# Optimization experiments

Hardware: AMD Instinct MI355X
Metric: run time of the kernel (lower is better)

## Reference

```python
import jax, jax.numpy as jnp
import numpy as np

OBJECTNESS_LIMIT = 0.7
MIN_SIZE = 10.0
N_ANCHORS = 9  # 3 aspects x 3 scales from RPN.anchors


def _conv(x, w, padding):
    return jax.lax.conv_general_dilated(
        x, w, window_strides=(1, 1), padding=padding,
        dimension_numbers=('NHWC', 'HWIO', 'NHWC'))


def setup_inputs() -> dict:
    key = jax.random.key(0)
    ks = jax.random.split(key, 7)
    B, H, W, C = 8, 64, 64, 512
    data = jax.random.normal(ks[0], (B, H, W, C), dtype=jnp.float32)
    # base 3x3 conv 512->256 ('normal' init), relu
    w_base = jax.random.normal(ks[1], (3, 3, C, 256), dtype=jnp.float32) * 0.05
    b_base = jnp.zeros((256,), dtype=jnp.float32)
    # classifier 1x1 conv 256->9 ('uniform' init), sigmoid
    w_cls = jax.random.uniform(ks[2], (1, 1, 256, N_ANCHORS), dtype=jnp.float32,
                               minval=-0.05, maxval=0.05)
    b_cls = jnp.zeros((N_ANCHORS,), dtype=jnp.float32)
    # branch is exercised / gradients flow)
    w_reg = jax.random.normal(ks[3], (1, 1, 256, N_ANCHORS * 4), dtype=jnp.float32) * 0.05
    b_reg = jnp.zeros((N_ANCHORS * 4,), dtype=jnp.float32)
    return {'data': data, 'w_base': w_base, 'b_base': b_base,
            'w_cls': w_cls, 'b_cls': b_cls, 'w_reg': w_reg, 'b_reg': b_reg}


def reference(data, w_base, b_base, w_cls, b_cls, w_reg, b_reg):
    # RPN base conv: 3x3, same padding, relu
    feat = jax.nn.relu(_conv(data, w_base, 'SAME') + b_base)        # [B,H,W,256]
    obj = jax.nn.sigmoid(_conv(feat, w_cls, 'VALID') + b_cls)       # [B,H,W,9]
    boxes = _conv(feat, w_reg, 'VALID') + b_reg                     # [B,H,W,36]
    B, H, W, _ = boxes.shape
    boxes = boxes.reshape(B, H, W, N_ANCHORS, 4)
    mask = (obj > OBJECTNESS_LIMIT) & (boxes[..., 2] > MIN_SIZE) & (boxes[..., 3] > MIN_SIZE)
    # boxes failing selection are dropped (yielded as None) -> zeroed here
    boxes = jnp.where(mask[..., None], boxes, jnp.zeros((), boxes.dtype))
    # objectness is always emitted; pack (boxes, objectness) densely
    out = jnp.concatenate([boxes.reshape(B, H, W, N_ANCHORS * 4), obj], axis=-1)  # [B,H,W,45]
    return out
```

## Files before the change

kernel.cpp:

```cpp
#include <hip/hip_runtime.h>
#include <hip/hip_bf16.h>

typedef unsigned short u16;
typedef unsigned int   u32;

typedef __attribute__((ext_vector_type(8))) short bfrag;
typedef __attribute__((ext_vector_type(4))) float f32x4;

static __device__ __forceinline__ u16 f2bf(float f) {
    u32 u = __float_as_uint(f);
    return (u16)((u + 0x7fffu + ((u >> 16) & 1u)) >> 16);
}
static __device__ __forceinline__ u32 pk2(float a, float b) {
    return (u32)f2bf(a) | ((u32)f2bf(b) << 16);
}
static __device__ __forceinline__ float bf2f(u16 h) {
    return __uint_as_float((u32)h << 16);
}

#define AS1 __attribute__((address_space(1)))
#define AS3 __attribute__((address_space(3)))
static __device__ __forceinline__ void gload_lds16(const u16* g, u16* l) {
    __builtin_amdgcn_global_load_lds((const AS1 u32*)g, (AS3 u32*)l, 16, 0, 0);
}

__global__ __launch_bounds__(256) void prep_w_k(const float* __restrict__ wb,
                                                u16* __restrict__ wt)
{
    int i  = blockIdx.x * 256 + threadIdx.x;
    int ci = i & 511;
    int co = (i >> 9) & 255;
    int pos = i >> 17;
    wt[i] = f2bf(wb[(size_t)((pos << 9) + ci) * 256 + co]);
}

__global__ __launch_bounds__(256) void prep_hw_k(const float* __restrict__ wc,
                                                 const float* __restrict__ wr,
                                                 u16* __restrict__ wh)
{
    int i = blockIdx.x * 256 + threadIdx.x;
    int ch = i >> 8, c = i & 255;
    float v = 0.f;
    if (ch < 36)      v = wr[c * 36 + ch];
    else if (ch < 45) v = wc[c * 9 + ch - 36];
    wh[i] = f2bf(v);
}

__global__ __launch_bounds__(256) void prep_a_k(const float* __restrict__ data,
                                                u16* __restrict__ abf)
{
    int gid = blockIdx.x * 256 + threadIdx.x;
    int ch8 = gid & 63;
    int row = gid >> 6;
    int img = row / 4356;
    int rem = row - img * 4356;
    int py  = rem / 66;
    int px  = rem - py * 66;
    uint4 o;
    if (py == 0 || py == 65 || px == 0 || px == 65) {
        o = make_uint4(0u, 0u, 0u, 0u);
    } else {
        const float4* s = (const float4*)(data +
            ((size_t)((img << 12) + ((py - 1) << 6) + (px - 1)) << 9) + (ch8 << 3));
        float4 v0 = s[0], v1 = s[1];
        o = make_uint4(pk2(v0.x, v0.y), pk2(v0.z, v0.w),
                       pk2(v1.x, v1.y), pk2(v1.z, v1.w));
    }
    *(uint4*)(abf + ((size_t)row << 9) + (ch8 << 3)) = o;
}

__global__ __launch_bounds__(256, 2) void gemm_k(
    const u16*   __restrict__ abf,
    const u16*   __restrict__ wt,
    const float* __restrict__ bb,
    u16*         __restrict__ feat)
{
    __shared__ u16 As[128 * 64];
    __shared__ u16 Bs[128 * 64];

    int bid = blockIdx.x;
    int wg  = ((bid & 7) << 6) | (bid >> 3);
    int mt  = wg >> 1, nt = wg & 1;
    int pm0 = mt << 7, cn0 = nt << 7;
    int img = mt >> 5;
    int y0  = (mt & 31) << 1;

    int tid = threadIdx.x, lane = tid & 63, w = tid >> 6;
    int wm2 = (w >> 1) << 6, wn2 = (w & 1) << 6;
    int fr = lane & 15, fg = lane >> 4;

    const u16* pA[4]; const u16* pB[4];
    int ldsOff[4];
    #pragma unroll
    for (int i = 0; i < 4; ++i) {
        int slot = i * 256 + w * 64 + lane;
        int row  = slot >> 3, g = slot & 7;
        int gs   = g ^ (row & 7);
        int y = y0 + (row >> 6), x = row & 63;
        pA[i] = abf + ((size_t)((img * 66 + y) * 66 + x) << 9) + (gs << 3);
        pB[i] = wt  + ((size_t)(cn0 + row) << 9) + (gs << 3);
        ldsOff[i] = (i * 256 + w * 64) << 3;
    }

    int aoff[2][4], boff[2][4];
    #pragma unroll
    for (int kk = 0; kk < 2; ++kk)
        #pragma unroll
        for (int t = 0; t < 4; ++t) {
            int ra = wm2 + (t << 4) + fr;
            int rb = wn2 + (t << 4) + fr;
            int q  = (kk << 2) | fg;
            aoff[kk][t] = (ra << 6) + ((q ^ (ra & 7)) << 3);
            boff[kk][t] = (rb << 6) + ((q ^ (rb & 7)) << 3);
        }

    f32x4 acc[4][4] = {};

    #pragma unroll 1
    for (int pos = 0; pos < 9; ++pos) {
        int py = pos / 3, px = pos % 3;
        size_t aEl = ((size_t)(py * 66 + px)) << 9;
        size_t bEl = ((size_t)pos) << 17;
        #pragma unroll 1
        for (int cb = 0; cb < 8; ++cb) {
            size_t soA = aEl + (cb << 6);
            size_t soB = bEl + (cb << 6);
            #pragma unroll
            for (int i = 0; i < 4; ++i) gload_lds16(pA[i] + soA, &As[ldsOff[i]]);
            #pragma unroll
            for (int i = 0; i < 4; ++i) gload_lds16(pB[i] + soB, &Bs[ldsOff[i]]);
            __syncthreads();

            #pragma unroll
            for (int kk = 0; kk < 2; ++kk) {
                bfrag av[4], bv[4];
                #pragma unroll
                for (int t = 0; t < 4; ++t) {
                    av[t] = *(const bfrag*)&As[aoff[kk][t]];
                    bv[t] = *(const bfrag*)&Bs[boff[kk][t]];
                }
                #pragma unroll
                for (int mi = 0; mi < 4; ++mi)
                    #pragma unroll
                    for (int ni = 0; ni < 4; ++ni)
                        acc[mi][ni] = __builtin_amdgcn_mfma_f32_16x16x32_bf16(
                            av[mi], bv[ni], acc[mi][ni], 0, 0, 0);
            }
            __syncthreads();
        }
    }

    #pragma unroll
    for (int ni = 0; ni < 4; ++ni) {
        int co = cn0 + wn2 + (ni << 4) + fr;
        float bias = bb[co];
        #pragma unroll
        for (int mi = 0; mi < 4; ++mi) {
            int pixb = pm0 + wm2 + (mi << 4) + (fg << 2);
            #pragma unroll
            for (int r = 0; r < 4; ++r) {
                float v = fmaxf(acc[mi][ni][r] + bias, 0.f);
                feat[(size_t)(pixb + r) * 256 + co] = f2bf(v);
            }
        }
    }
}

__global__ __launch_bounds__(256, 2) void head_k(
    const u16*   __restrict__ feat,
    const u16*   __restrict__ wh,
    const float* __restrict__ bc,
    const float* __restrict__ br,
    float*       __restrict__ out)
{
    __shared__ union {
        u16   ft[64 * 256];
        float raw[64 * 45];
    } sm;

    int bid = blockIdx.x;
    int wg  = ((bid & 7) << 6) | (bid >> 3);
    int pb  = wg << 6;

    int tid = threadIdx.x, lane = tid & 63, w = tid >> 6;
    int fr = lane & 15, fg = lane >> 4;
    int wm = w << 4;

    bfrag bv[3][8];
    #pragma unroll
    for (int nt = 0; nt < 3; ++nt)
        #pragma unroll
        for (int kk = 0; kk < 8; ++kk)
            bv[nt][kk] = *(const bfrag*)(wh + ((nt << 4) + fr) * 256 + (kk << 5) + (fg << 3));

    const u16* fbase = feat + ((size_t)pb << 8);
    #pragma unroll
    for (int i = 0; i < 8; ++i) {
        int slot = i * 256 + tid;
        int row  = slot >> 5, g = slot & 31;
        int gs   = g ^ (row & 7);
        gload_lds16(fbase + (row << 8) + (gs << 3), &sm.ft[(i * 256 + w * 64) << 3]);
    }
    __syncthreads();

    f32x4 acc[3] = {};
    #pragma unroll
    for (int kk = 0; kk < 8; ++kk) {
        int row = wm + fr;
        int ga  = (kk << 2) | fg;
        bfrag av = *(const bfrag*)&sm.ft[(row << 8) + ((ga ^ (row & 7)) << 3)];
        #pragma unroll
        for (int nt = 0; nt < 3; ++nt)
            acc[nt] = __builtin_amdgcn_mfma_f32_16x16x32_bf16(av, bv[nt][kk], acc[nt], 0, 0, 0);
    }
    __syncthreads();

    #pragma unroll
    for (int nt = 0; nt < 3; ++nt) {
        int ch = (nt << 4) + fr;
        if (ch < 45) {
            float bias = (ch < 36) ? br[ch] : bc[ch - 36];
            int pix = wm + (fg << 2);
            #pragma unroll
            for (int r = 0; r < 4; ++r)
                sm.raw[(pix + r) * 45 + ch] = acc[nt][r] + bias;
        }
    }
    __syncthreads();

    {
        int pix = tid >> 2, q = tid & 3;
        const float* rp = &sm.raw[pix * 45];
        float* op = out + (size_t)(pb + pix) * 45;
        int na = (q == 3) ? 3 : 2;
        int a0 = (q == 3) ? 6 : (q << 1);
        for (int t = 0; t < na; ++t) {
            int a = a0 + t;
            float lg  = rp[36 + a];
            float obj = 1.f / (1.f + __expf(-lg));
            float b0 = rp[4*a], b1 = rp[4*a+1], b2 = rp[4*a+2], b3 = rp[4*a+3];
            bool m = (obj > 0.7f) && (b2 > 10.f) && (b3 > 10.f);
            op[4*a    ] = m ? b0 : 0.f;
            op[4*a + 1] = m ? b1 : 0.f;
            op[4*a + 2] = m ? b2 : 0.f;
            op[4*a + 3] = m ? b3 : 0.f;
            op[36 + a ] = obj;
        }
    }
}

union FbSmem {
    u16   hal[3 * 66 * 64];
    u16   ft[256][64];
    float raw[64 * 45];
};

template<int WMODE>
__global__ __launch_bounds__(256, 2) void fb_k(
    const float* __restrict__ data, const u16* __restrict__ wt,
    const float* __restrict__ wb, const float* __restrict__ bb,
    const float* __restrict__ wc, const float* __restrict__ bc,
    const float* __restrict__ wr, const float* __restrict__ br,
    float* __restrict__ out)
{
    __shared__ FbSmem sm;
    int bid = blockIdx.x;
    int wg  = ((bid & 7) << 6) | (bid >> 3);
    int pm0 = wg << 6;
    int img = wg >> 6;
    int y0  = wg & 63;
    int tid = threadIdx.x, lane = tid & 63, wid = tid >> 6;
    int wn = wid << 6;
    int fr = lane & 15, fg = lane >> 4;
    f32x4 acc[4][4] = {};

    #pragma unroll 1
    for (int cb = 0; cb < 8; ++cb) {
        __syncthreads();
        #pragma unroll
        for (int t = 0; t < 3; ++t) {
            int lin = t * 256 + tid;
            int row = lin >> 8, col = (lin >> 2) & 63, cq = lin & 3;
            int sy = y0 + row - 1;
            bool ok = (sy >= 0) && (sy < 64);
            float4 v0, v1, v2, v3;
            if (ok) {
                const float4* s = (const float4*)(data +
                    ((size_t)((img << 12) + (sy << 6) + col) << 9) + (cb << 6) + (cq << 4));
                v0 = s[0]; v1 = s[1]; v2 = s[2]; v3 = s[3];
            } else { v0 = v1 = v2 = v3 = make_float4(0.f, 0.f, 0.f, 0.f); }
            int hc = col + 1;
            u16* base = &sm.hal[(row * 66 + hc) << 6];
            int g0 = ((cq << 1) | 0) ^ (hc & 7);
            int g1 = ((cq << 1) | 1) ^ (hc & 7);
            *(uint4*)&base[g0 << 3] = make_uint4(pk2(v0.x,v0.y), pk2(v0.z,v0.w),
                                                 pk2(v1.x,v1.y), pk2(v1.z,v1.w));
            *(uint4*)&base[g1 << 3] = make_uint4(pk2(v2.x,v2.y), pk2(v2.z,v2.w),
                                                 pk2(v3.x,v3.y), pk2(v3.z,v3.w));
        }
        if (tid < 48) {
            int zr = tid >> 4, zrem = tid & 15;
            int zc = (zrem >> 3) ? 65 : 0, zg = zrem & 7;
            *(uint4*)&sm.hal[(((zr * 66 + zc) << 3) | zg) << 3] = make_uint4(0,0,0,0);
        }
        __syncthreads();

        #pragma unroll
        for (int pos = 0; pos < 9; ++pos) {
            int dy = pos / 3 - 1, dx = pos % 3 - 1;
            bfrag bv[2][4];
            if (WMODE == 0) {
                #pragma unroll
                for (int kk = 0; kk < 2; ++kk)
                    #pragma unroll
                    for (int i = 0; i < 4; ++i)
                        bv[kk][i] = *(const bfrag*)(wt + ((size_t)pos << 17) +
                            ((size_t)(wn + (i << 4) + fr) << 9) + (cb << 6) +
                            (kk << 5) + (fg << 3));
            } else {
                #pragma unroll
                for (int kk = 0; kk < 2; ++kk)
                    #pragma unroll
                    for (int i = 0; i < 4; ++i) {
                        int co = wn + (i << 4) + fr;
                        const float* s = wb +
                            (size_t)((pos << 9) + (cb << 6) + (kk << 5) + (fg << 3)) * 256 + co;
                        union { short sh[8]; bfrag v; } tb;
                        #pragma unroll
                        for (int j = 0; j < 8; ++j) tb.sh[j] = (short)f2bf(s[(size_t)j << 8]);
                        bv[kk][i] = tb.v;
                    }
            }
            int hr = dy + 1;
            bfrag av[2][4];
            #pragma unroll
            for (int kk = 0; kk < 2; ++kk)
                #pragma unroll
                for (int i = 0; i < 4; ++i) {
                    int hc = (i << 4) + fr + dx + 1;
                    int g  = ((kk << 2) | fg) ^ (hc & 7);
                    av[kk][i] = *(const bfrag*)&sm.hal[(((hr * 66 + hc) << 3) | g) << 3];
                }
            #pragma unroll
            for (int kk = 0; kk < 2; ++kk)
                #pragma unroll
                for (int mi = 0; mi < 4; ++mi)
                    #pragma unroll
                    for (int ni = 0; ni < 4; ++ni)
                        acc[mi][ni] = __builtin_amdgcn_mfma_f32_16x16x32_bf16(
                            av[kk][mi], bv[kk][ni], acc[mi][ni], 0, 0, 0);
        }
    }
    __syncthreads();

    #pragma unroll
    for (int ni = 0; ni < 4; ++ni) {
        int co = wn + (ni << 4) + fr;
        float bias = bb[co];
        int rot = (co & 15) << 2;
        #pragma unroll
        for (int mi = 0; mi < 4; ++mi) {
            int pb  = (mi << 4) + (fg << 2);
            int col = (pb + rot) & 63;
            float r0 = fmaxf(acc[mi][ni][0] + bias, 0.f);
            float r1 = fmaxf(acc[mi][ni][1] + bias, 0.f);
            float r2 = fmaxf(acc[mi][ni][2] + bias, 0.f);
            float r3 = fmaxf(acc[mi][ni][3] + bias, 0.f);
            *(uint2*)&sm.ft[co][col] = make_uint2(pk2(r0, r1), pk2(r2, r3));
        }
    }
    __syncthreads();

    int wchx = __builtin_amdgcn_readfirstlane(wid) * 12;
    float a12[12];
    #pragma unroll
    for (int j = 0; j < 12; ++j) {
        int ch = wchx + j;
        a12[j] = (ch < 36) ? br[ch] : ((ch < 45) ? bc[ch - 36] : 0.f);
    }
    #pragma unroll 4
    for (int c = 0; c < 256; ++c) {
        int col = (lane + ((c & 15) << 2)) & 63;
        float f = bf2f(sm.ft[c][col]);
        #pragma unroll
        for (int j = 0; j < 12; ++j) {
            int ch = wchx + j;
            if (ch < 36)      a12[j] = fmaf(f, wr[c * 36 + ch], a12[j]);
            else if (ch < 45) a12[j] = fmaf(f, wc[c * 9 + ch - 36], a12[j]);
        }
    }
    __syncthreads();
    #pragma unroll
    for (int j = 0; j < 12; ++j) {
        int ch = wchx + j;
        if (ch < 45) sm.raw[lane * 45 + ch] = a12[j];
    }
    __syncthreads();
    {
        int pix = tid >> 2, q = tid & 3;
        const float* rp = &sm.raw[pix * 45];
        float* op = out + (size_t)(pm0 + pix) * 45;
        int na = (q == 3) ? 3 : 2;
        int a0 = (q == 3) ? 6 : (q << 1);
        for (int t = 0; t < na; ++t) {
            int a = a0 + t;
            float lg  = rp[36 + a];
            float obj = 1.f / (1.f + __expf(-lg));
            float b0 = rp[4*a], b1 = rp[4*a+1], b2 = rp[4*a+2], b3 = rp[4*a+3];
            bool m = (obj > 0.7f) && (b2 > 10.f) && (b3 > 10.f);
            op[4*a    ] = m ? b0 : 0.f;
            op[4*a + 1] = m ? b1 : 0.f;
            op[4*a + 2] = m ? b2 : 0.f;
            op[4*a + 3] = m ? b3 : 0.f;
            op[36 + a ] = obj;
        }
    }
}

extern "C" void kernel_launch(void* const* d_in, const int* in_sizes, int n_in,
                              void* d_out, int out_size, void* d_ws, size_t ws_size,
                              hipStream_t stream)
{
    const float* data = (const float*)d_in[0];
    const float* wb   = (const float*)d_in[1];
    const float* bb   = (const float*)d_in[2];
    const float* wc   = (const float*)d_in[3];
    const float* bcl  = (const float*)d_in[4];
    const float* wr   = (const float*)d_in[5];
    const float* brg  = (const float*)d_in[6];
    float* out = (float*)d_out;

    const size_t ABF_B  = (size_t)8 * 66 * 66 * 512 * 2;
    const size_t WT_B   = (size_t)9 * 256 * 512 * 2;
    const size_t FEAT_B = (size_t)32768 * 256 * 2;
    const size_t WH_B   = (size_t)64 * 256 * 2;

    if (ws_size >= ABF_B + WT_B + FEAT_B + WH_B) {
        u16* abf  = (u16*)d_ws;
        u16* wt   = (u16*)((char*)d_ws + ABF_B);
        u16* feat = (u16*)((char*)d_ws + ABF_B + WT_B);
        u16* wh   = (u16*)((char*)d_ws + ABF_B + WT_B + FEAT_B);
        prep_a_k<<<8712, 256, 0, stream>>>(data, abf);
        prep_w_k<<<4608, 256, 0, stream>>>(wb, wt);
        prep_hw_k<<<64, 256, 0, stream>>>(wc, wr, wh);
        gemm_k<<<512, 256, 0, stream>>>(abf, wt, bb, feat);
        head_k<<<512, 256, 0, stream>>>(feat, wh, bcl, brg, out);
    } else if (ws_size >= WT_B) {
        u16* wt = (u16*)d_ws;
        prep_w_k<<<4608, 256, 0, stream>>>(wb, wt);
        fb_k<0><<<512, 256, 0, stream>>>(data, wt, wb, bb, wc, bcl, wr, brg, out);
    } else {
        fb_k<1><<<512, 256, 0, stream>>>(data, (const u16*)nullptr, wb,
                                         bb, wc, bcl, wr, brg, out);
    }
}
```

Baseline: 114.6 us.

## Double GEMM K-tile to 128 and merge prep kernels into one launch

The three preprocessing kernels (activation pad/convert, base weight transpose, head weight pack) are merged into one launch that dispatches on block index, removing two kernel launches. The main conv GEMM K-step grows from 64 to 128 channels per stage, which halves the number of barrier pairs (72 to 36 iterations), and the loop order changes to channel-block outer, tap inner. LDS use doubles to 64 KB per block, which may limit occupancy to fewer blocks per CU and lengthens each exposed load-then-compute phase, since there is still no double buffering.

Result: faster. 105.9 us (-7.6%).

```diff
diff --git a/kernel.cpp b/kernel.cpp
--- a/kernel.cpp
+++ b/kernel.cpp
@@ -24,49 +24,49 @@
     __builtin_amdgcn_global_load_lds((const AS1 u32*)g, (AS3 u32*)l, 16, 0, 0);
 }
 
-__global__ __launch_bounds__(256) void prep_w_k(const float* __restrict__ wb,
-                                                u16* __restrict__ wt)
-{
-    int i  = blockIdx.x * 256 + threadIdx.x;
-    int ci = i & 511;
-    int co = (i >> 9) & 255;
-    int pos = i >> 17;
-    wt[i] = f2bf(wb[(size_t)((pos << 9) + ci) * 256 + co]);
-}
-
-__global__ __launch_bounds__(256) void prep_hw_k(const float* __restrict__ wc,
-                                                 const float* __restrict__ wr,
-                                                 u16* __restrict__ wh)
-{
-    int i = blockIdx.x * 256 + threadIdx.x;
-    int ch = i >> 8, c = i & 255;
-    float v = 0.f;
-    if (ch < 36)      v = wr[c * 36 + ch];
-    else if (ch < 45) v = wc[c * 9 + ch - 36];
-    wh[i] = f2bf(v);
-}
-
-__global__ __launch_bounds__(256) void prep_a_k(const float* __restrict__ data,
-                                                u16* __restrict__ abf)
-{
-    int gid = blockIdx.x * 256 + threadIdx.x;
-    int ch8 = gid & 63;
-    int row = gid >> 6;
-    int img = row / 4356;
-    int rem = row - img * 4356;
-    int py  = rem / 66;
-    int px  = rem - py * 66;
-    uint4 o;
-    if (py == 0 || py == 65 || px == 0 || px == 65) {
-        o = make_uint4(0u, 0u, 0u, 0u);
+__global__ __launch_bounds__(256) void prep_all_k(
+    const float* __restrict__ data,
+    const float* __restrict__ wb,
+    const float* __restrict__ wc,
+    const float* __restrict__ wr,
+    u16* __restrict__ abf,
+    u16* __restrict__ wt,
+    u16* __restrict__ wh)
+{
+    int b = blockIdx.x, tid = threadIdx.x;
+    if (b < 8712) {
+        int gid = b * 256 + tid;
+        int ch8 = gid & 63;
+        int row = gid >> 6;
+        int img = row / 4356;
+        int rem = row - img * 4356;
+        int py  = rem / 66;
+        int px  = rem - py * 66;
+        uint4 o;
+        if (py == 0 || py == 65 || px == 0 || px == 65) {
+            o = make_uint4(0u, 0u, 0u, 0u);
+        } else {
+            const float4* s = (const float4*)(data +
+                ((size_t)((img << 12) + ((py - 1) << 6) + (px - 1)) << 9) + (ch8 << 3));
+            float4 v0 = s[0], v1 = s[1];
+            o = make_uint4(pk2(v0.x, v0.y), pk2(v0.z, v0.w),
+                           pk2(v1.x, v1.y), pk2(v1.z, v1.w));
+        }
+        *(uint4*)(abf + ((size_t)row << 9) + (ch8 << 3)) = o;
+    } else if (b < 13320) {
+        int i  = (b - 8712) * 256 + tid;
+        int ci = i & 511;
+        int co = (i >> 9) & 255;
+        int pos = i >> 17;
+        wt[i] = f2bf(wb[(size_t)((pos << 9) + ci) * 256 + co]);
     } else {
-        const float4* s = (const float4*)(data +
-            ((size_t)((img << 12) + ((py - 1) << 6) + (px - 1)) << 9) + (ch8 << 3));
-        float4 v0 = s[0], v1 = s[1];
-        o = make_uint4(pk2(v0.x, v0.y), pk2(v0.z, v0.w),
-                       pk2(v1.x, v1.y), pk2(v1.z, v1.w));
-    }
-    *(uint4*)(abf + ((size_t)row << 9) + (ch8 << 3)) = o;
+        int i = (b - 13320) * 256 + tid;
+        int ch = i >> 8, c = i & 255;
+        float v = 0.f;
+        if (ch < 36)      v = wr[c * 36 + ch];
+        else if (ch < 45) v = wc[c * 9 + ch - 36];
+        wh[i] = f2bf(v);
+    }
 }
 
 __global__ __launch_bounds__(256, 2) void gemm_k(
@@ -75,8 +75,8 @@
     const float* __restrict__ bb,
     u16*         __restrict__ feat)
 {
-    __shared__ u16 As[128 * 64];
-    __shared__ u16 Bs[128 * 64];
+    __shared__ u16 As[128 * 128];
+    __shared__ u16 Bs[128 * 128];
 
     int bid = blockIdx.x;
     int wg  = ((bid & 7) << 6) | (bid >> 3);
@@ -89,12 +89,12 @@
     int wm2 = (w >> 1) << 6, wn2 = (w & 1) << 6;
     int fr = lane & 15, fg = lane >> 4;
 
-    const u16* pA[4]; const u16* pB[4];
-    int ldsOff[4];
-    #pragma unroll
-    for (int i = 0; i < 4; ++i) {
+    const u16* pA[8]; const u16* pB[8];
+    int ldsOff[8];
+    #pragma unroll
+    for (int i = 0; i < 8; ++i) {
         int slot = i * 256 + w * 64 + lane;
-        int row  = slot >> 3, g = slot & 7;
+        int row  = slot >> 4, g = slot & 15;
         int gs   = g ^ (row & 7);
         int y = y0 + (row >> 6), x = row & 63;
         pA[i] = abf + ((size_t)((img * 66 + y) * 66 + x) << 9) + (gs << 3);
@@ -102,37 +102,36 @@
         ldsOff[i] = (i * 256 + w * 64) << 3;
     }
 
-    int aoff[2][4], boff[2][4];
-    #pragma unroll
-    for (int kk = 0; kk < 2; ++kk)
+    int aoff[4][4], boff[4][4];
+    #pragma unroll
+    for (int kk = 0; kk < 4; ++kk)
         #pragma unroll
         for (int t = 0; t < 4; ++t) {
             int ra = wm2 + (t << 4) + fr;
             int rb = wn2 + (t << 4) + fr;
             int q  = (kk << 2) | fg;
-            aoff[kk][t] = (ra << 6) + ((q ^ (ra & 7)) << 3);
-            boff[kk][t] = (rb << 6) + ((q ^ (rb & 7)) << 3);
+            aoff[kk][t] = (ra << 7) + ((q ^ (ra & 7)) << 3);
+            boff[kk][t] = (rb << 7) + ((q ^ (rb & 7)) << 3);
         }
 
     f32x4 acc[4][4] = {};
 
     #pragma unroll 1
-    for (int pos = 0; pos < 9; ++pos) {
-        int py = pos / 3, px = pos % 3;
-        size_t aEl = ((size_t)(py * 66 + px)) << 9;
-        size_t bEl = ((size_t)pos) << 17;
+    for (int kb = 0; kb < 4; ++kb) {
+        size_t kOff = (size_t)(kb << 7);
         #pragma unroll 1
-        for (int cb = 0; cb < 8; ++cb) {
-            size_t soA = aEl + (cb << 6);
-            size_t soB = bEl + (cb << 6);
-            #pragma unroll
-            for (int i = 0; i < 4; ++i) gload_lds16(pA[i] + soA, &As[ldsOff[i]]);
-            #pragma unroll
-            for (int i = 0; i < 4; ++i) gload_lds16(pB[i] + soB, &Bs[ldsOff[i]]);
+        for (int pos = 0; pos < 9; ++pos) {
+            int py = pos / 3, px = pos % 3;
+            size_t soA = (((size_t)(py * 66 + px)) << 9) + kOff;
+            size_t soB = (((size_t)pos) << 17) + kOff;
+            #pragma unroll
+            for (int i = 0; i < 8; ++i) gload_lds16(pA[i] + soA, &As[ldsOff[i]]);
+            #pragma unroll
+            for (int i = 0; i < 8; ++i) gload_lds16(pB[i] + soB, &Bs[ldsOff[i]]);
             __syncthreads();
 
             #pragma unroll
-            for (int kk = 0; kk < 2; ++kk) {
+            for (int kk = 0; kk < 4; ++kk) {
                 bfrag av[4], bv[4];
                 #pragma unroll
                 for (int t = 0; t < 4; ++t) {
@@ -247,6 +246,16 @@
             op[36 + a ] = obj;
         }
     }
+}
+
+__global__ __launch_bounds__(256) void prep_w_k(const float* __restrict__ wb,
+                                                u16* __restrict__ wt)
+{
+    int i  = blockIdx.x * 256 + threadIdx.x;
+    int ci = i & 511;
+    int co = (i >> 9) & 255;
+    int pos = i >> 17;
+    wt[i] = f2bf(wb[(size_t)((pos << 9) + ci) * 256 + co]);
 }
 
 union FbSmem {
@@ -440,9 +449,7 @@
         u16* wt   = (u16*)((char*)d_ws + ABF_B);
         u16* feat = (u16*)((char*)d_ws + ABF_B + WT_B);
         u16* wh   = (u16*)((char*)d_ws + ABF_B + WT_B + FEAT_B);
-        prep_a_k<<<8712, 256, 0, stream>>>(data, abf);
-        prep_w_k<<<4608, 256, 0, stream>>>(wb, wt);
-        prep_hw_k<<<64, 256, 0, stream>>>(wc, wr, wh);
+        prep_all_k<<<13384, 256, 0, stream>>>(data, wb, wc, wr, abf, wt, wh);
         gemm_k<<<512, 256, 0, stream>>>(abf, wt, bb, feat);
         head_k<<<512, 256, 0, stream>>>(feat, wh, bcl, brg, out);
     } else if (ws_size >= WT_B) {
```
